# Optimization experiments

Hardware: AMD Instinct MI355X
Metric: run time of the kernel (lower is better)

Reference implementation:

```python
import jax, jax.numpy as jnp
import numpy as np

DEGREES = [1, 2, 3, 4]
REPEATS = np.array([2 * l + 1 for l in DEGREES])  # [3,5,7,9]
M_TOT = int(REPEATS.sum())  # 24
NUM_DEGREES = len(DEGREES)
SEG_IDS = np.repeat(np.arange(NUM_DEGREES), REPEATS)  # (M_TOT,)
# One-hot segment matrix: P[m, l] = 1 if component m belongs to degree l.
# (ev*ev) @ P  == per-degree segment_sum of squares (L0 contraction)
# cev @ P.T    == per-degree repeat back to m_tot components
P_NP = np.eye(NUM_DEGREES, dtype=np.float32)[SEG_IDS]  # (M_TOT, NUM_DEGREES)

N = 500_000
F = 132  # num_features
D_IN = F + NUM_DEGREES  # 136 (Dense in = out)


def setup_inputs() -> dict:
    key = jax.random.key(0)
    k1, k2, k3 = jax.random.split(key, 3)
    x = jax.random.normal(k1, (N, F), dtype=jnp.float32)
    ev = jax.random.normal(k2, (N, M_TOT), dtype=jnp.float32)
    # lecun_normal kernel for Dense(features=F+num_degrees)
    W = jax.random.normal(k3, (D_IN, D_IN), dtype=jnp.float32) / jnp.sqrt(D_IN)
    b = jnp.zeros((D_IN,), dtype=jnp.float32)
    return {"x": x, "ev": ev, "W": W, "b": b}


def reference(x, ev, W, b):
    P = jnp.asarray(P_NP, dtype=x.dtype)
    # L0 contraction: per-degree sum of squares over 2l+1 components -> (N, num_degrees)
    contr = (ev * ev) @ P
    y = jnp.concatenate([x, contr], axis=-1) @ W + b  # (N, F + num_degrees)
    cx = y[:, :F]            # (N, F)
    cev = y[:, F:]           # (N, num_degrees)
    # degree-repeat cev to (N, m_tot) and gate ev
    return cx, (cev @ P.T) * ev
```

## Files before the change

kernel.cpp:

```cpp
#include <hip/hip_runtime.h>
#include <stdint.h>

#define NROWS 500000
#define FDIM 132

typedef unsigned short u16;
typedef unsigned int   u32;

typedef __attribute__((ext_vector_type(8))) u16    us8;
typedef __attribute__((ext_vector_type(4))) u16    us4;
typedef __attribute__((ext_vector_type(8))) __bf16 bf16x8;
typedef __attribute__((ext_vector_type(4))) float  f32x4;

__device__ __forceinline__ u16 f2bf(float f) {
    u32 u = __builtin_bit_cast(u32, f);
    u = u + 0x7FFFu + ((u >> 16) & 1u);
    return (u16)(u >> 16);
}
__device__ __forceinline__ float bf2f(u16 h) {
    return __builtin_bit_cast(float, (u32)h << 16);
}

__global__ __launch_bounds__(256) void wconv_kernel(const float* __restrict__ W,
                                                    u16* __restrict__ wt) {
    int id = blockIdx.x * 256 + threadIdx.x;
    int n = id >> 7, k = id & 127;
    float v = (n < 136) ? W[k * 136 + n] : 0.0f;
    wt[id] = f2bf(v);
}

__global__ __launch_bounds__(256, 2) void exch_kernel(const float* __restrict__ x,
                                                      const float* __restrict__ ev,
                                                      const float* __restrict__ W,
                                                      const float* __restrict__ b,
                                                      const u16* __restrict__ wt,
                                                      float* __restrict__ out) {
    __shared__ __align__(16) u16   Wt_sh[144 * 128];
    __shared__ __align__(16) u16   A_sh[64 * 128];
    __shared__ __align__(16) float Wtl_sh[8 * 136];
    __shared__ __align__(16) float ev_sh[64 * 24];
    __shared__ __align__(16) u16   xt_sh[64 * 4];
    __shared__ __align__(16) float contr_sh[64 * 4];

    const int tid  = threadIdx.x;
    const int row0 = blockIdx.x * 64;

#pragma unroll
    for (int i = 0; i < 9; ++i) {
        int c = tid + i * 256;
        us8 v = *(const us8*)(wt + c * 8);
        int n = c >> 4, ch = c & 15;
        int phys = ch ^ (n & 7);
        *(us8*)(&Wt_sh[n * 128 + phys * 8]) = v;
    }

#pragma unroll
    for (int i = 0; i < 4; ++i) {
        int c = tid + i * 256;
        int row = c >> 4, ch = c & 15;
        int grow = row0 + row;
        f32x4 a0 = {0.f, 0.f, 0.f, 0.f}, a1 = {0.f, 0.f, 0.f, 0.f};
        if (grow < NROWS) {
            const float* p = x + (size_t)grow * FDIM + ch * 8;
            a0 = *(const f32x4*)p;
            a1 = *(const f32x4*)(p + 4);
        }
        us8 v;
        v[0] = f2bf(a0[0]); v[1] = f2bf(a0[1]); v[2] = f2bf(a0[2]); v[3] = f2bf(a0[3]);
        v[4] = f2bf(a1[0]); v[5] = f2bf(a1[1]); v[6] = f2bf(a1[2]); v[7] = f2bf(a1[3]);
        int phys = ch ^ (row & 7);
        *(us8*)(&A_sh[row * 128 + phys * 8]) = v;
    }

    if (tid < 64) {
        int grow = row0 + tid;
        f32x4 a = {0.f, 0.f, 0.f, 0.f};
        if (grow < NROWS) a = *(const f32x4*)(x + (size_t)grow * FDIM + 128);
        us4 v;
        v[0] = f2bf(a[0]); v[1] = f2bf(a[1]); v[2] = f2bf(a[2]); v[3] = f2bf(a[3]);
        *(us4*)(&xt_sh[tid * 4]) = v;
    }

#pragma unroll
    for (int i = 0; i < 2; ++i) {
        int c = tid + i * 256;
        if (c < 384) {
            int row = c / 6, j4 = c % 6;
            int grow = row0 + row;
            f32x4 e = {0.f, 0.f, 0.f, 0.f};
            if (grow < NROWS) e = *(const f32x4*)(ev + (size_t)grow * 24 + j4 * 4);
            *(f32x4*)(&ev_sh[row * 24 + j4 * 4]) = e;
        }
    }

    {
        int c = tid;
        f32x4 v = *(const f32x4*)(W + 128 * 136 + c * 4);
        *(f32x4*)(&Wtl_sh[c * 4]) = v;
        if (tid < 16) {
            int c2 = tid + 256;
            f32x4 v2 = *(const f32x4*)(W + 128 * 136 + c2 * 4);
            *(f32x4*)(&Wtl_sh[c2 * 4]) = v2;
        }
    }

    __syncthreads();

    {
        int r = tid >> 2, d = tid & 3;
        int st = d * (d + 2);
        int len = 2 * d + 3;
        float s = 0.f;
        for (int j = 0; j < len; ++j) {
            float v = ev_sh[r * 24 + st + j];
            s += v * v;
        }
        contr_sh[r * 4 + d] = s;
    }

    const int lane = tid & 63;
    const int w    = tid >> 6;
    const int ln   = lane & 15;
    const int q    = lane >> 4;

    f32x4 acc[9];
#pragma unroll
    for (int t = 0; t < 9; ++t) acc[t] = (f32x4){0.f, 0.f, 0.f, 0.f};

#pragma unroll
    for (int kc = 0; kc < 4; ++kc) {
        int phys = (kc * 4 + q) ^ (ln & 7);
        int off  = ln * 128 + phys * 8;
        bf16x8 a = __builtin_bit_cast(bf16x8, *(const us8*)(&A_sh[w * 2048 + off]));
#pragma unroll
        for (int t = 0; t < 9; ++t) {
            bf16x8 bb = __builtin_bit_cast(bf16x8, *(const us8*)(&Wt_sh[t * 2048 + off]));
            acc[t] = __builtin_amdgcn_mfma_f32_16x16x32_bf16(a, bb, acc[t], 0, 0, 0);
        }
    }

    __syncthreads();

    float xtv[4][4], cv[4][4];
#pragma unroll
    for (int r = 0; r < 4; ++r) {
        int row = w * 16 + q * 4 + r;
        us4 xr = *(const us4*)(&xt_sh[row * 4]);
#pragma unroll
        for (int i = 0; i < 4; ++i) xtv[r][i] = bf2f(xr[i]);
        f32x4 c4 = *(const f32x4*)(&contr_sh[row * 4]);
#pragma unroll
        for (int d = 0; d < 4; ++d) cv[r][d] = c4[d];
    }

#pragma unroll
    for (int t = 0; t < 9; ++t) {
        int col = t * 16 + ln;
        float wt8[8];
        float bias = 0.f;
        if (col < 136) {
#pragma unroll
            for (int i = 0; i < 8; ++i) wt8[i] = Wtl_sh[i * 136 + col];
            bias = b[col];
        } else {
#pragma unroll
            for (int i = 0; i < 8; ++i) wt8[i] = 0.f;
        }
#pragma unroll
        for (int r = 0; r < 4; ++r) {
            float y = acc[t][r] + bias;
#pragma unroll
            for (int i = 0; i < 4; ++i) y += xtv[r][i] * wt8[i];
#pragma unroll
            for (int d = 0; d < 4; ++d) y += cv[r][d] * wt8[4 + d];
            acc[t][r] = y;
        }
    }

    __syncthreads();

#pragma unroll
    for (int t = 0; t < 9; ++t) {
        int col = t * 16 + ln;
#pragma unroll
        for (int r = 0; r < 4; ++r) {
            int row  = w * 16 + q * 4 + r;
            int grow = row0 + row;
            float y  = acc[t][r];
            if (col < FDIM) {
                if (grow < NROWS) out[(size_t)grow * FDIM + col] = y;
            } else if (col < 136) {
                contr_sh[row * 4 + (col - FDIM)] = y;
            }
        }
    }

    __syncthreads();

#pragma unroll
    for (int i = 0; i < 2; ++i) {
        int c = tid + i * 256;
        if (c < 384) {
            int row = c / 6, j4 = c % 6;
            int grow = row0 + row;
            if (grow < NROWS) {
                f32x4 e = *(const f32x4*)(&ev_sh[row * 24 + j4 * 4]);
                f32x4 o;
#pragma unroll
                for (int u = 0; u < 4; ++u) {
                    int m = j4 * 4 + u;
                    int d = (m < 3) ? 0 : (m < 8) ? 1 : (m < 15) ? 2 : 3;
                    o[u] = contr_sh[row * 4 + d] * e[u];
                }
                *(f32x4*)(out + (size_t)NROWS * FDIM + (size_t)grow * 24 + j4 * 4) = o;
            }
        }
    }
}

extern "C" void kernel_launch(void* const* d_in, const int* in_sizes, int n_in,
                              void* d_out, int out_size, void* d_ws, size_t ws_size,
                              hipStream_t stream) {
    const float* x  = (const float*)d_in[0];
    const float* ev = (const float*)d_in[1];
    const float* W  = (const float*)d_in[2];
    const float* b  = (const float*)d_in[3];
    u16* wt = (u16*)d_ws;

    wconv_kernel<<<72, 256, 0, stream>>>(W, wt);
    int nblk = (NROWS + 63) / 64;
    exch_kernel<<<nblk, 256, 0, stream>>>(x, ev, W, b, wt, (float*)d_out);
}
```

Before: 600.0 us.

## Make exchange kernel persistent with async global-to-LDS prefetch of next tile

Replaces the one-block-per-tile launch with a persistent grid of 768 blocks that loop over 64-row tiles. The next tile's x and ev are prefetched straight into LDS with global_load_lds DMA while the current tile is still in its epilogue, and ev is double-buffered. The bf16 weight matrix is no longer staged in LDS; B fragments are read from global/L2 each k-step, and x is held as fp32 in LDS and converted to bf16 at fragment load. Work is split so wave pairs share rows and divide the output column tiles. This aims to hide load latency and cut per-block setup, at the cost of repeated global weight reads and a single A buffer, which forces the prefetch to wait until all MFMA reads of the current tile are done.

```diff
diff --git a/kernel.cpp b/kernel.cpp
--- a/kernel.cpp
+++ b/kernel.cpp
@@ -3,23 +3,27 @@
 
 #define NROWS 500000
 #define FDIM 132
+#define NTILES 7813
+#define GRID 768
 
 typedef unsigned short u16;
 typedef unsigned int   u32;
 
 typedef __attribute__((ext_vector_type(8))) u16    us8;
-typedef __attribute__((ext_vector_type(4))) u16    us4;
 typedef __attribute__((ext_vector_type(8))) __bf16 bf16x8;
 typedef __attribute__((ext_vector_type(4))) float  f32x4;
+
+typedef __attribute__((address_space(1))) const void* as1_cvp;
+typedef __attribute__((address_space(3))) void*       as3_vp;
 
 __device__ __forceinline__ u16 f2bf(float f) {
     u32 u = __builtin_bit_cast(u32, f);
     u = u + 0x7FFFu + ((u >> 16) & 1u);
     return (u16)(u >> 16);
 }
-__device__ __forceinline__ float bf2f(u16 h) {
-    return __builtin_bit_cast(float, (u32)h << 16);
-}
+
+#define BAR_FULL() asm volatile("s_waitcnt vmcnt(0) lgkmcnt(0)\n\ts_barrier" ::: "memory")
+#define BAR_LDS()  asm volatile("s_waitcnt lgkmcnt(0)\n\ts_barrier" ::: "memory")
 
 __global__ __launch_bounds__(256) void wconv_kernel(const float* __restrict__ W,
                                                     u16* __restrict__ wt) {
@@ -29,192 +33,198 @@
     wt[id] = f2bf(v);
 }
 
-__global__ __launch_bounds__(256, 2) void exch_kernel(const float* __restrict__ x,
+__global__ __launch_bounds__(256, 3) void exch_kernel(const float* __restrict__ x,
                                                       const float* __restrict__ ev,
                                                       const float* __restrict__ W,
                                                       const float* __restrict__ b,
                                                       const u16* __restrict__ wt,
                                                       float* __restrict__ out) {
-    __shared__ __align__(16) u16   Wt_sh[144 * 128];
-    __shared__ __align__(16) u16   A_sh[64 * 128];
+    __shared__ __align__(16) float A_sh[64 * 132];
+    __shared__ __align__(16) float ev_sh[2][64 * 24];
     __shared__ __align__(16) float Wtl_sh[8 * 136];
-    __shared__ __align__(16) float ev_sh[64 * 24];
-    __shared__ __align__(16) u16   xt_sh[64 * 4];
+    __shared__ __align__(16) float b_sh[136];
+    __shared__ __align__(16) float xt_sh[64 * 4];
     __shared__ __align__(16) float contr_sh[64 * 4];
-
-    const int tid  = threadIdx.x;
-    const int row0 = blockIdx.x * 64;
-
-#pragma unroll
-    for (int i = 0; i < 9; ++i) {
-        int c = tid + i * 256;
-        us8 v = *(const us8*)(wt + c * 8);
-        int n = c >> 4, ch = c & 15;
-        int phys = ch ^ (n & 7);
-        *(us8*)(&Wt_sh[n * 128 + phys * 8]) = v;
-    }
-
-#pragma unroll
-    for (int i = 0; i < 4; ++i) {
-        int c = tid + i * 256;
-        int row = c >> 4, ch = c & 15;
-        int grow = row0 + row;
-        f32x4 a0 = {0.f, 0.f, 0.f, 0.f}, a1 = {0.f, 0.f, 0.f, 0.f};
-        if (grow < NROWS) {
-            const float* p = x + (size_t)grow * FDIM + ch * 8;
-            a0 = *(const f32x4*)p;
-            a1 = *(const f32x4*)(p + 4);
-        }
-        us8 v;
-        v[0] = f2bf(a0[0]); v[1] = f2bf(a0[1]); v[2] = f2bf(a0[2]); v[3] = f2bf(a0[3]);
-        v[4] = f2bf(a1[0]); v[5] = f2bf(a1[1]); v[6] = f2bf(a1[2]); v[7] = f2bf(a1[3]);
-        int phys = ch ^ (row & 7);
-        *(us8*)(&A_sh[row * 128 + phys * 8]) = v;
-    }
-
-    if (tid < 64) {
-        int grow = row0 + tid;
-        f32x4 a = {0.f, 0.f, 0.f, 0.f};
-        if (grow < NROWS) a = *(const f32x4*)(x + (size_t)grow * FDIM + 128);
-        us4 v;
-        v[0] = f2bf(a[0]); v[1] = f2bf(a[1]); v[2] = f2bf(a[2]); v[3] = f2bf(a[3]);
-        *(us4*)(&xt_sh[tid * 4]) = v;
-    }
-
-#pragma unroll
-    for (int i = 0; i < 2; ++i) {
-        int c = tid + i * 256;
-        if (c < 384) {
-            int row = c / 6, j4 = c % 6;
-            int grow = row0 + row;
-            f32x4 e = {0.f, 0.f, 0.f, 0.f};
-            if (grow < NROWS) e = *(const f32x4*)(ev + (size_t)grow * 24 + j4 * 4);
-            *(f32x4*)(&ev_sh[row * 24 + j4 * 4]) = e;
-        }
-    }
-
-    {
-        int c = tid;
-        f32x4 v = *(const f32x4*)(W + 128 * 136 + c * 4);
-        *(f32x4*)(&Wtl_sh[c * 4]) = v;
-        if (tid < 16) {
-            int c2 = tid + 256;
-            f32x4 v2 = *(const f32x4*)(W + 128 * 136 + c2 * 4);
-            *(f32x4*)(&Wtl_sh[c2 * 4]) = v2;
-        }
-    }
-
-    __syncthreads();
-
-    {
-        int r = tid >> 2, d = tid & 3;
-        int st = d * (d + 2);
-        int len = 2 * d + 3;
-        float s = 0.f;
-        for (int j = 0; j < len; ++j) {
-            float v = ev_sh[r * 24 + st + j];
-            s += v * v;
-        }
-        contr_sh[r * 4 + d] = s;
-    }
-
-    const int lane = tid & 63;
-    const int w    = tid >> 6;
-    const int ln   = lane & 15;
-    const int q    = lane >> 4;
-
-    f32x4 acc[9];
-#pragma unroll
-    for (int t = 0; t < 9; ++t) acc[t] = (f32x4){0.f, 0.f, 0.f, 0.f};
-
-#pragma unroll
-    for (int kc = 0; kc < 4; ++kc) {
-        int phys = (kc * 4 + q) ^ (ln & 7);
-        int off  = ln * 128 + phys * 8;
-        bf16x8 a = __builtin_bit_cast(bf16x8, *(const us8*)(&A_sh[w * 2048 + off]));
-#pragma unroll
-        for (int t = 0; t < 9; ++t) {
-            bf16x8 bb = __builtin_bit_cast(bf16x8, *(const us8*)(&Wt_sh[t * 2048 + off]));
-            acc[t] = __builtin_amdgcn_mfma_f32_16x16x32_bf16(a, bb, acc[t], 0, 0, 0);
-        }
-    }
-
-    __syncthreads();
-
-    float xtv[4][4], cv[4][4];
-#pragma unroll
-    for (int r = 0; r < 4; ++r) {
-        int row = w * 16 + q * 4 + r;
-        us4 xr = *(const us4*)(&xt_sh[row * 4]);
-#pragma unroll
-        for (int i = 0; i < 4; ++i) xtv[r][i] = bf2f(xr[i]);
-        f32x4 c4 = *(const f32x4*)(&contr_sh[row * 4]);
-#pragma unroll
-        for (int d = 0; d < 4; ++d) cv[r][d] = c4[d];
-    }
-
-#pragma unroll
-    for (int t = 0; t < 9; ++t) {
-        int col = t * 16 + ln;
-        float wt8[8];
-        float bias = 0.f;
-        if (col < 136) {
-#pragma unroll
-            for (int i = 0; i < 8; ++i) wt8[i] = Wtl_sh[i * 136 + col];
-            bias = b[col];
-        } else {
-#pragma unroll
-            for (int i = 0; i < 8; ++i) wt8[i] = 0.f;
-        }
-#pragma unroll
-        for (int r = 0; r < 4; ++r) {
-            float y = acc[t][r] + bias;
-#pragma unroll
-            for (int i = 0; i < 4; ++i) y += xtv[r][i] * wt8[i];
-#pragma unroll
-            for (int d = 0; d < 4; ++d) y += cv[r][d] * wt8[4 + d];
-            acc[t][r] = y;
-        }
-    }
-
-    __syncthreads();
-
-#pragma unroll
-    for (int t = 0; t < 9; ++t) {
-        int col = t * 16 + ln;
-#pragma unroll
-        for (int r = 0; r < 4; ++r) {
-            int row  = w * 16 + q * 4 + r;
-            int grow = row0 + row;
-            float y  = acc[t][r];
-            if (col < FDIM) {
-                if (grow < NROWS) out[(size_t)grow * FDIM + col] = y;
-            } else if (col < 136) {
-                contr_sh[row * 4 + (col - FDIM)] = y;
-            }
-        }
-    }
-
-    __syncthreads();
-
-#pragma unroll
-    for (int i = 0; i < 2; ++i) {
-        int c = tid + i * 256;
-        if (c < 384) {
-            int row = c / 6, j4 = c % 6;
-            int grow = row0 + row;
-            if (grow < NROWS) {
-                f32x4 e = *(const f32x4*)(&ev_sh[row * 24 + j4 * 4]);
-                f32x4 o;
-#pragma unroll
-                for (int u = 0; u < 4; ++u) {
-                    int m = j4 * 4 + u;
-                    int d = (m < 3) ? 0 : (m < 8) ? 1 : (m < 15) ? 2 : 3;
-                    o[u] = contr_sh[row * 4 + d] * e[u];
+    __shared__ __align__(16) float cev_sh[64 * 4];
+
+    const int tid   = threadIdx.x;
+    const int lane  = tid & 63;
+    const int w     = tid >> 6;
+    const int c     = w & 1;
+    const int rbase = (w >> 1) * 32;
+    const int ln    = lane & 15;
+    const int q     = lane >> 4;
+    const int tbase = c ? 5 : 0;
+
+    for (int c0 = tid; c0 < 272; c0 += 256)
+        *(f32x4*)(&Wtl_sh[c0 * 4]) = *(const f32x4*)(W + 128 * 136 + c0 * 4);
+    if (tid < 34)
+        *(f32x4*)(&b_sh[tid * 4]) = *(const f32x4*)(b + tid * 4);
+
+    auto dma_tile = [&](int tile, int pbuf) {
+        int row0 = tile * 64;
+        int vr   = NROWS - row0; if (vr > 64) vr = 64;
+        int vbA  = vr * 528;
+        int vbE  = vr * 96;
+        const char* xg = (const char*)(x + (size_t)row0 * FDIM);
+        const char* eg = (const char*)(ev + (size_t)row0 * 24);
+        char* Ab = (char*)A_sh;
+        char* Eb = (char*)ev_sh[pbuf];
+#pragma unroll
+        for (int ii = 0; ii < 9; ++ii) {
+            int i = w + ii * 4;
+            if (i < 33) {
+                int off = i * 1024 + lane * 16;
+                if (off + 16 <= vbA)
+                    __builtin_amdgcn_global_load_lds((as1_cvp)(xg + off),
+                                                     (as3_vp)(Ab + i * 1024), 16, 0, 0);
+            }
+        }
+#pragma unroll
+        for (int ii = 0; ii < 2; ++ii) {
+            int i = w + ii * 4;
+            if (i < 6) {
+                int off = i * 1024 + lane * 16;
+                if (off + 16 <= vbE)
+                    __builtin_amdgcn_global_load_lds((as1_cvp)(eg + off),
+                                                     (as3_vp)(Eb + i * 1024), 16, 0, 0);
+            }
+        }
+    };
+
+    int p = 0;
+    dma_tile(blockIdx.x, 0);
+
+    for (int tile = blockIdx.x; tile < NTILES; tile += GRID) {
+        const int row0 = tile * 64;
+        const float* evp = ev_sh[p];
+
+        BAR_FULL();
+
+        {
+            int r = tid >> 2, d = tid & 3;
+            int st = d * (d + 2);
+            int len = 2 * d + 3;
+            float s = 0.f;
+            for (int j = 0; j < len; ++j) {
+                float v = evp[r * 24 + st + j];
+                s += v * v;
+            }
+            contr_sh[r * 4 + d] = s;
+            xt_sh[tid] = A_sh[r * FDIM + 128 + d];
+        }
+
+        f32x4 acc[2][5];
+#pragma unroll
+        for (int s2 = 0; s2 < 2; ++s2)
+#pragma unroll
+            for (int i = 0; i < 5; ++i) acc[s2][i] = (f32x4){0.f, 0.f, 0.f, 0.f};
+
+#pragma unroll
+        for (int kc = 0; kc < 4; ++kc) {
+            us8 bf[5];
+#pragma unroll
+            for (int i = 0; i < 5; ++i) {
+                int t = tbase + i;
+                if (t < 9)
+                    bf[i] = *(const us8*)(wt + (size_t)(t * 16 + ln) * 128 + kc * 32 + q * 8);
+            }
+#pragma unroll
+            for (int sub = 0; sub < 2; ++sub) {
+                const float* ap = &A_sh[(rbase + sub * 16 + ln) * FDIM + kc * 32 + q * 8];
+                f32x4 a0 = *(const f32x4*)ap;
+                f32x4 a1 = *(const f32x4*)(ap + 4);
+                us8 av;
+                av[0] = f2bf(a0[0]); av[1] = f2bf(a0[1]); av[2] = f2bf(a0[2]); av[3] = f2bf(a0[3]);
+                av[4] = f2bf(a1[0]); av[5] = f2bf(a1[1]); av[6] = f2bf(a1[2]); av[7] = f2bf(a1[3]);
+                bf16x8 a16 = __builtin_bit_cast(bf16x8, av);
+#pragma unroll
+                for (int i = 0; i < 5; ++i) {
+                    int t = tbase + i;
+                    if (t < 9)
+                        acc[sub][i] = __builtin_amdgcn_mfma_f32_16x16x32_bf16(
+                            a16, __builtin_bit_cast(bf16x8, bf[i]), acc[sub][i], 0, 0, 0);
                 }
-                *(f32x4*)(out + (size_t)NROWS * FDIM + (size_t)grow * 24 + j4 * 4) = o;
-            }
-        }
+            }
+        }
+
+        BAR_LDS();
+
+        {
+            int nxt = tile + GRID;
+            if (nxt < NTILES) dma_tile(nxt, p ^ 1);
+        }
+
+        float wt8v[5][8], biasv[5];
+#pragma unroll
+        for (int i = 0; i < 5; ++i) {
+            int t = tbase + i;
+            int col = t * 16 + ln;
+            if (t < 9 && col < 136) {
+#pragma unroll
+                for (int j = 0; j < 8; ++j) wt8v[i][j] = Wtl_sh[j * 136 + col];
+                biasv[i] = b_sh[col];
+            } else {
+#pragma unroll
+                for (int j = 0; j < 8; ++j) wt8v[i][j] = 0.f;
+                biasv[i] = 0.f;
+            }
+        }
+#pragma unroll
+        for (int sub = 0; sub < 2; ++sub) {
+            f32x4 xr[4], cr[4];
+#pragma unroll
+            for (int r = 0; r < 4; ++r) {
+                int row = rbase + sub * 16 + q * 4 + r;
+                xr[r] = *(const f32x4*)(&xt_sh[row * 4]);
+                cr[r] = *(const f32x4*)(&contr_sh[row * 4]);
+            }
+#pragma unroll
+            for (int i = 0; i < 5; ++i) {
+                int t = tbase + i;
+                if (t >= 9) continue;
+                int col = t * 16 + ln;
+#pragma unroll
+                for (int r = 0; r < 4; ++r) {
+                    int row  = rbase + sub * 16 + q * 4 + r;
+                    int grow = row0 + row;
+                    float y = acc[sub][i][r] + biasv[i];
+                    y += xr[r][0] * wt8v[i][0] + xr[r][1] * wt8v[i][1]
+                       + xr[r][2] * wt8v[i][2] + xr[r][3] * wt8v[i][3];
+                    y += cr[r][0] * wt8v[i][4] + cr[r][1] * wt8v[i][5]
+                       + cr[r][2] * wt8v[i][6] + cr[r][3] * wt8v[i][7];
+                    if (col < FDIM) {
+                        if (grow < NROWS) out[(size_t)grow * FDIM + col] = y;
+                    } else if (col < 136) {
+                        cev_sh[row * 4 + (col - FDIM)] = y;
+                    }
+                }
+            }
+        }
+
+        BAR_LDS();
+
+#pragma unroll
+        for (int i2 = 0; i2 < 2; ++i2) {
+            int cix = tid + i2 * 256;
+            if (cix < 384) {
+                int row = cix / 6, j4 = cix % 6;
+                int grow = row0 + row;
+                if (grow < NROWS) {
+                    f32x4 e = *(const f32x4*)(&evp[row * 24 + j4 * 4]);
+                    f32x4 o;
+#pragma unroll
+                    for (int u = 0; u < 4; ++u) {
+                        int m = j4 * 4 + u;
+                        int d = (m < 3) ? 0 : (m < 8) ? 1 : (m < 15) ? 2 : 3;
+                        o[u] = cev_sh[row * 4 + d] * e[u];
+                    }
+                    *(f32x4*)(out + (size_t)NROWS * FDIM + (size_t)grow * 24 + j4 * 4) = o;
+                }
+            }
+        }
+
+        p ^= 1;
     }
 }
 
@@ -228,6 +238,5 @@
     u16* wt = (u16*)d_ws;
 
     wconv_kernel<<<72, 256, 0, stream>>>(W, wt);
-    int nblk = (NROWS + 63) / 64;
-    exch_kernel<<<nblk, 256, 0, stream>>>(x, ev, W, b, wt, (float*)d_out);
-}
+    exch_kernel<<<GRID, 256, 0, stream>>>(x, ev, W, b, wt, (float*)d_out);
+}
```

Result: slower. 847.6 us (+41.3%).
